# Kernel tuning notes

Hardware: AMD Instinct MI355X
Metric: run time of the kernel (lower is better)

Reference implementation:

```python
import jax, jax.numpy as jnp
import numpy as np

LOG2PI = float(np.log(2.0 * np.pi))
Q_LOGVAR = float(np.log(0.25))  # log(0.5^2)


def _kld(mu, logvar, q_mu, q_logvar):
    return -0.5 * (1.0 + logvar - q_logvar
                   - (jnp.square(mu - q_mu) + jnp.exp(logvar)) / jnp.exp(q_logvar))


def _log_normal(x):
    return -0.5 * (LOG2PI + jnp.square(x))


def setup_inputs() -> dict:
    key = jax.random.key(0)
    ks = jax.random.split(key, 10)
    N, D, E = 8192, 64, 262144
    return {
        "z_mu_n": jax.random.normal(ks[0], (N, D), jnp.float32),
        "z_logvar_n": jax.random.normal(ks[1], (N, D), jnp.float32),
        "z_mu_e": jax.random.normal(ks[2], (N, D), jnp.float32),
        "z_logvar_e": jax.random.normal(ks[3], (N, D), jnp.float32),
        "Alpha_mu": jax.random.normal(ks[4], (D,), jnp.float32),
        "Beta_mu": jax.random.normal(ks[5], (D,), jnp.float32),
        "edge_logits": jax.random.normal(ks[6], (N, N), jnp.float32),
        "mu_Alpha": jax.random.normal(ks[7], (D,), jnp.float32),
        "mu_Beta": jax.random.normal(ks[8], (D,), jnp.float32),
        "edge_index": jax.random.randint(ks[9], (2, E), 0, N, jnp.int64),
        "num_nodes": N,
    }


def reference(z_mu_n, z_logvar_n, z_mu_e, z_logvar_e, Alpha_mu, Beta_mu,
              edge_logits, mu_Alpha, mu_Beta, edge_index, num_nodes):
    N = num_nodes
    i, j = edge_index[0], edge_index[1]
    # single fused symmetric scatter replacing the per-edge Python loop
    adj = jnp.zeros((N, N), jnp.float32).at[i, j].set(1.0).at[j, i].set(1.0)

    # BCEWithLogitsLoss (mean reduction), numerically stable
    x = edge_logits
    logpx_z = jnp.mean(jnp.maximum(x, 0.0) - x * adj + jnp.log1p(jnp.exp(-jnp.abs(x))))

    Alpha_logvar = jnp.full_like(Alpha_mu, Q_LOGVAR)
    Beta_logvar = jnp.full_like(Beta_mu, Q_LOGVAR)

    log_pmu_Alpha = jnp.mean(_log_normal(mu_Alpha))
    log_pmu_Beta = jnp.mean(_log_normal(mu_Beta))

    extra_kl_Alpha = jnp.mean(_kld(mu_Alpha, Alpha_logvar, Alpha_mu, Alpha_logvar))
    extra_kl_Beta = jnp.mean(_kld(mu_Beta, Beta_logvar, Beta_mu, Beta_logvar))

    # [N, D] latents broadcast against [D] prior params
    kl_structure = jnp.mean(_kld(z_mu_e, z_logvar_e, mu_Alpha, Q_LOGVAR))
    kl_semantic = jnp.mean(_kld(z_mu_n, z_logvar_n, mu_Beta, Q_LOGVAR))

    return (log_pmu_Alpha + extra_kl_Alpha + log_pmu_Beta + extra_kl_Beta
            + logpx_z + kl_structure + kl_semantic)
```

## Files before the change

kernel.cpp:

```cpp
#include <hip/hip_runtime.h>


static constexpr double D_LOG2PI = 1.8378770664093453;
static constexpr float  KL_C0    = -1.1931471805599453f;

__device__ __forceinline__ void block_reduce_add(double v, double* acc) {
#pragma unroll
  for (int off = 32; off > 0; off >>= 1)
    v += __shfl_down(v, off, 64);
  __shared__ double s[8];
  const int lane = threadIdx.x & 63;
  const int wv   = threadIdx.x >> 6;
  if (lane == 0) s[wv] = v;
  __syncthreads();
  if (threadIdx.x == 0) {
    double t = s[0];
    const int nw = (blockDim.x + 63) >> 6;
    for (int w = 1; w < nw; ++w) t += s[w];
    atomicAdd(acc, t);
  }
}

__device__ __forceinline__ float softplus_fast(float x) {
  const float t = __builtin_amdgcn_exp2f(-1.442695041f * fabsf(x));
  return fmaxf(x, 0.f) + 0.6931471806f * __builtin_amdgcn_logf(1.f + t);
}

__global__ __launch_bounds__(64) void k_init(double* __restrict__ accs,
                                             int* __restrict__ flag,
                                             const int* __restrict__ eidx) {
  const int t = threadIdx.x;
  if (t < 8) accs[t] = 0.0;
  const int w = eidx[2 * t + 1];
  const unsigned long long m = __ballot(w == 0);
  if (t == 0) *flag = (m == 0xFFFFFFFFFFFFFFFFull) ? 1 : 0;
}

__global__ __launch_bounds__(256) void k_main(
    const float4* __restrict__ x4, long long n4,
    const int* __restrict__ eidx, const float* __restrict__ x, int N, int E,
    const int* __restrict__ flag,
    const float4* __restrict__ zmu_n, const float4* __restrict__ zlv_n,
    const float4* __restrict__ zmu_e, const float4* __restrict__ zlv_e,
    const float4* __restrict__ muA, const float4* __restrict__ muB,
    long long nd4, int d4mask,
    double* __restrict__ accs, int spB, int edB) {
  const int b = blockIdx.x;
  if (b < spB) {
    long long i = (long long)b * blockDim.x + threadIdx.x;
    const long long stride = (long long)spB * blockDim.x;
    double local = 0.0;
    for (; i < n4; i += stride) {
      const float4 v = x4[i];
      float s = softplus_fast(v.x) + softplus_fast(v.y)
              + softplus_fast(v.z) + softplus_fast(v.w);
      local += (double)s;
    }
    block_reduce_add(local, accs + 0);
  } else if (b < spB + edB) {
    const int is64 = *flag;
    const long long t0 = (long long)(b - spB) * blockDim.x + threadIdx.x;
    const long long stride = (long long)edB * blockDim.x;
    double local = 0.0;
    for (long long e = t0; e < E; e += stride) {
      int i, j;
      if (is64) {
        i = eidx[2 * e];
        j = eidx[2 * ((long long)E + e)];
      } else {
        i = eidx[e];
        j = eidx[(long long)E + e];
      }
      float v = x[(long long)i * N + j];
      if (i != j) v += x[(long long)j * N + i];
      local += (double)v;
    }
    block_reduce_add(local, accs + 1);
  } else {
    long long i = (long long)(b - spB - edB) * blockDim.x + threadIdx.x;
    const long long stride = (long long)(gridDim.x - spB - edB) * blockDim.x;
    double local = 0.0;
    for (; i < nd4; i += stride) {
      const int dv = (int)(i & d4mask);
      const float4 qa = muA[dv];
      const float4 qb = muB[dv];
      const float4 me = zmu_e[i];
      const float4 le = zlv_e[i];
      const float4 mn = zmu_n[i];
      const float4 ln_ = zlv_n[i];
      float s = 0.f;
      {
        float d0 = me.x - qa.x, d1 = me.y - qa.y, d2 = me.z - qa.z, d3 = me.w - qa.w;
        s += KL_C0 - 0.5f * le.x + 2.f * (d0 * d0 + __expf(le.x));
        s += KL_C0 - 0.5f * le.y + 2.f * (d1 * d1 + __expf(le.y));
        s += KL_C0 - 0.5f * le.z + 2.f * (d2 * d2 + __expf(le.z));
        s += KL_C0 - 0.5f * le.w + 2.f * (d3 * d3 + __expf(le.w));
      }
      {
        float d0 = mn.x - qb.x, d1 = mn.y - qb.y, d2 = mn.z - qb.z, d3 = mn.w - qb.w;
        s += KL_C0 - 0.5f * ln_.x + 2.f * (d0 * d0 + __expf(ln_.x));
        s += KL_C0 - 0.5f * ln_.y + 2.f * (d1 * d1 + __expf(ln_.y));
        s += KL_C0 - 0.5f * ln_.z + 2.f * (d2 * d2 + __expf(ln_.z));
        s += KL_C0 - 0.5f * ln_.w + 2.f * (d3 * d3 + __expf(ln_.w));
      }
      local += (double)s;
    }
    block_reduce_add(local, accs + 2);
  }
}

__global__ __launch_bounds__(64) void k_final(const float* __restrict__ Alpha_mu,
                                              const float* __restrict__ Beta_mu,
                                              const float* __restrict__ mu_A,
                                              const float* __restrict__ mu_B,
                                              const double* __restrict__ accs,
                                              float* __restrict__ out,
                                              int D, double invN2, double invND) {
  const int d = threadIdx.x;
  double t = 0.0;
  if (d < D) {
    const double ma = mu_A[d], mb = mu_B[d];
    const double aa = Alpha_mu[d], bb = Beta_mu[d];
    t = -0.5 * (D_LOG2PI + ma * ma) + 2.0 * (ma - aa) * (ma - aa)
      + -0.5 * (D_LOG2PI + mb * mb) + 2.0 * (mb - bb) * (mb - bb);
  }
#pragma unroll
  for (int off = 32; off > 0; off >>= 1)
    t += __shfl_down(t, off, 64);
  if (d == 0) {
    const double r = (accs[0] - accs[1]) * invN2
                   + accs[2] * invND
                   + t / (double)D;
    out[0] = (float)r;
  }
}

extern "C" void kernel_launch(void* const* d_in, const int* in_sizes, int n_in,
                              void* d_out, int out_size, void* d_ws, size_t ws_size,
                              hipStream_t stream) {
  const float* z_mu_n   = (const float*)d_in[0];
  const float* z_lv_n   = (const float*)d_in[1];
  const float* z_mu_e   = (const float*)d_in[2];
  const float* z_lv_e   = (const float*)d_in[3];
  const float* Alpha_mu = (const float*)d_in[4];
  const float* Beta_mu  = (const float*)d_in[5];
  const float* elog     = (const float*)d_in[6];
  const float* mu_A     = (const float*)d_in[7];
  const float* mu_B     = (const float*)d_in[8];
  const int*   eidx     = (const int*)d_in[9];

  const int D = in_sizes[4];
  const int N = in_sizes[0] / D;
  const int E = in_sizes[9] / 2;
  const long long N2 = (long long)N * N;
  const long long ND = (long long)N * D;

  double* accs = (double*)d_ws;
  int* flag = (int*)(accs + 8);
  float* out = (float*)d_out;

  const int spB = 4096, edB = 1024, klB = 256;

  k_init<<<1, 64, 0, stream>>>(accs, flag, eidx);
  k_main<<<spB + edB + klB, 256, 0, stream>>>(
      (const float4*)elog, N2 / 4,
      eidx, elog, N, E, flag,
      (const float4*)z_mu_n, (const float4*)z_lv_n,
      (const float4*)z_mu_e, (const float4*)z_lv_e,
      (const float4*)mu_A, (const float4*)mu_B,
      ND / 4, D / 4 - 1,
      accs, spB, edB);
  k_final<<<1, 64, 0, stream>>>(Alpha_mu, Beta_mu, mu_A, mu_B, accs, out,
                                D, 1.0 / (double)N2, 1.0 / (double)ND);
}
```

Before: 404.4 us.

## Replace global atomics with per-block partials and drop init kernel

Each block now writes its reduced partial sum to its own workspace slot instead of doing a double-precision atomicAdd, and a 1024-thread final kernel sums and weights all partials. The separate init kernel is gone: edge blocks recompute the int64-layout flag with a wave ballot, and accumulators no longer need zeroing. The softplus loop is unrolled 4x to put more loads in flight, and edge and KL block counts are halved. Together these cut one launch and the atomic contention, at the cost of a larger final reduction and redundant flag loads per edge block.

```diff
diff --git a/kernel.cpp b/kernel.cpp
--- a/kernel.cpp
+++ b/kernel.cpp
@@ -4,61 +4,53 @@
 static constexpr double D_LOG2PI = 1.8378770664093453;
 static constexpr float  KL_C0    = -1.1931471805599453f;
 
-__device__ __forceinline__ void block_reduce_add(double v, double* acc) {
-#pragma unroll
-  for (int off = 32; off > 0; off >>= 1)
-    v += __shfl_down(v, off, 64);
-  __shared__ double s[8];
-  const int lane = threadIdx.x & 63;
-  const int wv   = threadIdx.x >> 6;
-  if (lane == 0) s[wv] = v;
-  __syncthreads();
-  if (threadIdx.x == 0) {
-    double t = s[0];
-    const int nw = (blockDim.x + 63) >> 6;
-    for (int w = 1; w < nw; ++w) t += s[w];
-    atomicAdd(acc, t);
-  }
-}
-
 __device__ __forceinline__ float softplus_fast(float x) {
   const float t = __builtin_amdgcn_exp2f(-1.442695041f * fabsf(x));
   return fmaxf(x, 0.f) + 0.6931471806f * __builtin_amdgcn_logf(1.f + t);
 }
 
-__global__ __launch_bounds__(64) void k_init(double* __restrict__ accs,
-                                             int* __restrict__ flag,
-                                             const int* __restrict__ eidx) {
-  const int t = threadIdx.x;
-  if (t < 8) accs[t] = 0.0;
-  const int w = eidx[2 * t + 1];
-  const unsigned long long m = __ballot(w == 0);
-  if (t == 0) *flag = (m == 0xFFFFFFFFFFFFFFFFull) ? 1 : 0;
+__device__ __forceinline__ float sp4(const float4 v) {
+  return softplus_fast(v.x) + softplus_fast(v.y)
+       + softplus_fast(v.z) + softplus_fast(v.w);
+}
+
+__device__ __forceinline__ void block_reduce_store(double v, double* slot) {
+#pragma unroll
+  for (int off = 32; off > 0; off >>= 1)
+    v += __shfl_down(v, off, 64);
+  __shared__ double s[4];
+  const int lane = threadIdx.x & 63;
+  const int wv   = threadIdx.x >> 6;
+  if (lane == 0) s[wv] = v;
+  __syncthreads();
+  if (threadIdx.x == 0) *slot = s[0] + s[1] + s[2] + s[3];
 }
 
 __global__ __launch_bounds__(256) void k_main(
     const float4* __restrict__ x4, long long n4,
     const int* __restrict__ eidx, const float* __restrict__ x, int N, int E,
-    const int* __restrict__ flag,
     const float4* __restrict__ zmu_n, const float4* __restrict__ zlv_n,
     const float4* __restrict__ zmu_e, const float4* __restrict__ zlv_e,
     const float4* __restrict__ muA, const float4* __restrict__ muB,
     long long nd4, int d4mask,
-    double* __restrict__ accs, int spB, int edB) {
+    double* __restrict__ partials, int spB, int edB) {
   const int b = blockIdx.x;
   if (b < spB) {
+    const long long S = (long long)spB * blockDim.x;
     long long i = (long long)b * blockDim.x + threadIdx.x;
-    const long long stride = (long long)spB * blockDim.x;
     double local = 0.0;
-    for (; i < n4; i += stride) {
-      const float4 v = x4[i];
-      float s = softplus_fast(v.x) + softplus_fast(v.y)
-              + softplus_fast(v.z) + softplus_fast(v.w);
-      local += (double)s;
+    for (; i + 3 * S < n4; i += 4 * S) {
+      const float4 a = x4[i];
+      const float4 c = x4[i + S];
+      const float4 d = x4[i + 2 * S];
+      const float4 e = x4[i + 3 * S];
+      local += (double)(sp4(a) + sp4(c) + sp4(d) + sp4(e));
     }
-    block_reduce_add(local, accs + 0);
+    for (; i < n4; i += S) local += (double)sp4(x4[i]);
+    block_reduce_store(local, partials + b);
   } else if (b < spB + edB) {
-    const int is64 = *flag;
+    const int w0 = eidx[2 * (threadIdx.x & 63) + 1];
+    const int is64 = (__ballot(w0 == 0) == 0xFFFFFFFFFFFFFFFFull) ? 1 : 0;
     const long long t0 = (long long)(b - spB) * blockDim.x + threadIdx.x;
     const long long stride = (long long)edB * blockDim.x;
     double local = 0.0;
@@ -75,7 +67,7 @@
       if (i != j) v += x[(long long)j * N + i];
       local += (double)v;
     }
-    block_reduce_add(local, accs + 1);
+    block_reduce_store(local, partials + b);
   } else {
     long long i = (long long)(b - spB - edB) * blockDim.x + threadIdx.x;
     const long long stride = (long long)(gridDim.x - spB - edB) * blockDim.x;
@@ -105,33 +97,41 @@
       }
       local += (double)s;
     }
-    block_reduce_add(local, accs + 2);
+    block_reduce_store(local, partials + b);
   }
 }
 
-__global__ __launch_bounds__(64) void k_final(const float* __restrict__ Alpha_mu,
-                                              const float* __restrict__ Beta_mu,
-                                              const float* __restrict__ mu_A,
-                                              const float* __restrict__ mu_B,
-                                              const double* __restrict__ accs,
-                                              float* __restrict__ out,
-                                              int D, double invN2, double invND) {
-  const int d = threadIdx.x;
-  double t = 0.0;
-  if (d < D) {
-    const double ma = mu_A[d], mb = mu_B[d];
-    const double aa = Alpha_mu[d], bb = Beta_mu[d];
-    t = -0.5 * (D_LOG2PI + ma * ma) + 2.0 * (ma - aa) * (ma - aa)
-      + -0.5 * (D_LOG2PI + mb * mb) + 2.0 * (mb - bb) * (mb - bb);
+__global__ __launch_bounds__(1024) void k_final(
+    const double* __restrict__ partials, int nB, int spB, int edB,
+    const float* __restrict__ Alpha_mu, const float* __restrict__ Beta_mu,
+    const float* __restrict__ mu_A, const float* __restrict__ mu_B,
+    float* __restrict__ out, int D, double invN2, double invND) {
+  const int tid = threadIdx.x;
+  double local = 0.0;
+  for (int b = tid; b < nB; b += 1024) {
+    const double w = (b < spB) ? invN2 : ((b < spB + edB) ? -invN2 : invND);
+    local += partials[b] * w;
+  }
+  if (tid < D) {
+    const double ma = mu_A[tid], mb = mu_B[tid];
+    const double aa = Alpha_mu[tid], bb = Beta_mu[tid];
+    const double t = -0.5 * (D_LOG2PI + ma * ma) + 2.0 * (ma - aa) * (ma - aa)
+                   + -0.5 * (D_LOG2PI + mb * mb) + 2.0 * (mb - bb) * (mb - bb);
+    local += t / (double)D;
   }
 #pragma unroll
   for (int off = 32; off > 0; off >>= 1)
-    t += __shfl_down(t, off, 64);
-  if (d == 0) {
-    const double r = (accs[0] - accs[1]) * invN2
-                   + accs[2] * invND
-                   + t / (double)D;
-    out[0] = (float)r;
+    local += __shfl_down(local, off, 64);
+  __shared__ double s[16];
+  const int lane = tid & 63;
+  const int wv   = tid >> 6;
+  if (lane == 0) s[wv] = local;
+  __syncthreads();
+  if (tid == 0) {
+    double t = 0.0;
+#pragma unroll
+    for (int w = 0; w < 16; ++w) t += s[w];
+    out[0] = (float)t;
   }
 }
 
@@ -155,21 +155,21 @@
   const long long N2 = (long long)N * N;
   const long long ND = (long long)N * D;
 
-  double* accs = (double*)d_ws;
-  int* flag = (int*)(accs + 8);
+  double* partials = (double*)d_ws;
   float* out = (float*)d_out;
 
-  const int spB = 4096, edB = 1024, klB = 256;
+  const int spB = 4096, edB = 512, klB = 128;
+  const int nB = spB + edB + klB;
 
-  k_init<<<1, 64, 0, stream>>>(accs, flag, eidx);
-  k_main<<<spB + edB + klB, 256, 0, stream>>>(
+  k_main<<<nB, 256, 0, stream>>>(
       (const float4*)elog, N2 / 4,
-      eidx, elog, N, E, flag,
+      eidx, elog, N, E,
       (const float4*)z_mu_n, (const float4*)z_lv_n,
       (const float4*)z_mu_e, (const float4*)z_lv_e,
       (const float4*)mu_A, (const float4*)mu_B,
       ND / 4, D / 4 - 1,
-      accs, spB, edB);
-  k_final<<<1, 64, 0, stream>>>(Alpha_mu, Beta_mu, mu_A, mu_B, accs, out,
-                                D, 1.0 / (double)N2, 1.0 / (double)ND);
+      partials, spB, edB);
+  k_final<<<1, 1024, 0, stream>>>(partials, nB, spB, edB,
+                                  Alpha_mu, Beta_mu, mu_A, mu_B, out,
+                                  D, 1.0 / (double)N2, 1.0 / (double)ND);
 }
```

Result: faster. 394.9 us (-2.4%).
